# Kernel optimization log

Hardware: AMD Instinct MI355X
Metric: run time of the kernel (lower is better)

## Reference

```python
import jax, jax.numpy as jnp
import numpy as np

B, N, C = 16, 8192, 384   # batch, points, feature dim
G, M = 512, 32            # num_group (FPS centers), group_size (KNN k)


def setup_inputs() -> dict:
    key = jax.random.key(0)
    k1, k2 = jax.random.split(key)
    xyz = jax.random.normal(k1, (B, N, 3), dtype=jnp.float32)
    features = jax.random.normal(k2, (B, N, C), dtype=jnp.float32)
    return {"xyz": xyz, "features": features}


def _fps(xyz, n_samples):
    """Farthest point sampling, deterministic start at index 0 (matches CUDA op).
    xyz: [B, N, 3] -> idx: [B, n_samples] int32."""
    b, n, _ = xyz.shape
    big = jnp.asarray(1e10, xyz.dtype)

    def step(carry, _):
        min_dist, farthest = carry
        centroid = jnp.take_along_axis(xyz, farthest[:, None, None], axis=1)  # [B,1,3]
        d = jnp.sum((xyz - centroid) ** 2, axis=-1)                            # [B,N]
        min_dist = jnp.minimum(min_dist, d)
        nxt = jnp.argmax(min_dist, axis=-1).astype(jnp.int32)
        return (min_dist, nxt), farthest

    init = (jnp.full((b, n), big, xyz.dtype), jnp.zeros((b,), jnp.int32))
    _, idxs = jax.lax.scan(step, init, None, length=n_samples)  # [G, B]
    return jnp.transpose(idxs)  # [B, G]


def _knn_idx(ref, query, k):
    """Indices of k nearest ref points for each query. ref [B,N,3], query [B,G,3] -> [B,G,k]."""
    d = (jnp.sum(query ** 2, -1)[..., None]
         + jnp.sum(ref ** 2, -1)[:, None, :]
         - 2.0 * jnp.einsum('bgd,bnd->bgn', query, ref))  # [B,G,N]
    _, idx = jax.lax.top_k(-d, k)
    return idx


def reference(xyz, features):
    fps_idx = _fps(xyz, G)                                        # [B,G]
    center = jnp.take_along_axis(xyz, fps_idx[..., None], axis=1)  # [B,G,3]
    idx = _knn_idx(xyz, center, M)                                 # [B,G,M]

    gather = jax.vmap(lambda pts, i: pts[i])                       # per-batch fancy gather
    flat_idx = idx.reshape(B, G * M)
    neighborhood = gather(xyz, flat_idx).reshape(B, G, M, 3)
    feature_group = gather(features, flat_idx).reshape(B, G, M, C)
    neighborhood = neighborhood - center[:, :, None, :]
    return neighborhood, center, feature_group
```

## Files before the change

### kernel.cpp

```cpp
#include <hip/hip_runtime.h>
#include <math.h>

#define BATCH 16
#define NPTS  8192
#define FEATC 384
#define NG    512
#define KM    32

#define OUT0_OFF 0
#define OUT1_OFF (BATCH * NG * KM * 3)
#define OUT2_OFF (OUT1_OFF + BATCH * NG * 3)

#pragma clang fp contract(off)

typedef float f32x2 __attribute__((ext_vector_type(2)));

template <int CTRL>
__device__ __forceinline__ unsigned long long dpp_u64(unsigned long long k) {
    unsigned lo = (unsigned)k, hi = (unsigned)(k >> 32);
    lo = (unsigned)__builtin_amdgcn_update_dpp((int)lo, (int)lo, CTRL, 0xF, 0xF, false);
    hi = (unsigned)__builtin_amdgcn_update_dpp((int)hi, (int)hi, CTRL, 0xF, 0xF, false);
    return ((unsigned long long)hi << 32) | lo;
}

__device__ __forceinline__ unsigned long long wave_max_u64(unsigned long long k) {
    unsigned long long o;
    o = dpp_u64<0x111>(k); if (o > k) k = o;
    o = dpp_u64<0x112>(k); if (o > k) k = o;
    o = dpp_u64<0x114>(k); if (o > k) k = o;
    o = dpp_u64<0x118>(k); if (o > k) k = o;
    o = dpp_u64<0x142>(k); if (o > k) k = o;
    o = dpp_u64<0x143>(k); if (o > k) k = o;
    return k;
}

__device__ __forceinline__ unsigned long long wave_min_u64(unsigned long long k) {
    unsigned long long o;
    o = dpp_u64<0x111>(k); if (o < k) k = o;
    o = dpp_u64<0x112>(k); if (o < k) k = o;
    o = dpp_u64<0x114>(k); if (o < k) k = o;
    o = dpp_u64<0x118>(k); if (o < k) k = o;
    o = dpp_u64<0x142>(k); if (o < k) k = o;
    o = dpp_u64<0x143>(k); if (o < k) k = o;
    return k;
}

__device__ __forceinline__ unsigned long long min16_u64(const unsigned long long* k) {
    unsigned long long t8[8];
#pragma unroll
    for (int i = 0; i < 8; ++i) t8[i] = k[i] < k[i + 8] ? k[i] : k[i + 8];
    unsigned long long t4[4];
#pragma unroll
    for (int i = 0; i < 4; ++i) t4[i] = t8[i] < t8[i + 4] ? t8[i] : t8[i + 4];
    unsigned long long a = t4[0] < t4[2] ? t4[0] : t4[2];
    unsigned long long b = t4[1] < t4[3] ? t4[1] : t4[3];
    return a < b ? a : b;
}

__global__ void init_progress(int* progress) {
    if (threadIdx.x < BATCH)
        __hip_atomic_store(&progress[threadIdx.x], 0,
                           __ATOMIC_RELAXED, __HIP_MEMORY_SCOPE_AGENT);
}

__global__ __launch_bounds__(512) void group_kernel(const float* __restrict__ xyz,
                                                    const float* __restrict__ features,
                                                    float* __restrict__ out0,
                                                    float* __restrict__ out1,
                                                    float* __restrict__ out2,
                                                    int* __restrict__ progress) {
#pragma clang fp contract(off)
    __shared__ unsigned long long sk[2][8];
    __shared__ int   sidx[KM];
    __shared__ float scst[24];

    const int tid  = threadIdx.x;
    const int lane = tid & 63;
    const int wid  = tid >> 6;

    if (blockIdx.x < BATCH) {
        __builtin_amdgcn_s_setprio(3);
        const int b = blockIdx.x;
        const float* xb = xyz + (size_t)b * NPTS * 3;
        float* co = out1 + (size_t)b * NG * 3;

        f32x2 X[8], Y[8], Z[8], MD[8];
#pragma unroll
        for (int j = 0; j < 8; ++j) {
            int p0 = tid + 1024 * j;
            int p1 = p0 + 512;
            X[j]  = (f32x2){xb[p0 * 3 + 0], xb[p1 * 3 + 0]};
            Y[j]  = (f32x2){xb[p0 * 3 + 1], xb[p1 * 3 + 1]};
            Z[j]  = (f32x2){xb[p0 * 3 + 2], xb[p1 * 3 + 2]};
            MD[j] = (f32x2){1e10f, 1e10f};
        }

        int far = 0;
        for (int g = 0; g < NG; ++g) {
            const float cx = xb[far * 3 + 0];
            const float cy = xb[far * 3 + 1];
            const float cz = xb[far * 3 + 2];
            if (tid == 0) {
                scst[(g & 7) * 3 + 0] = cx;
                scst[(g & 7) * 3 + 1] = cy;
                scst[(g & 7) * 3 + 2] = cz;
            }
            const f32x2 cx2 = (f32x2){cx, cx};
            const f32x2 cy2 = (f32x2){cy, cy};
            const f32x2 cz2 = (f32x2){cz, cz};

#pragma unroll
            for (int j = 0; j < 8; ++j) {
                f32x2 dx = X[j] - cx2;
                f32x2 dy = Y[j] - cy2;
                f32x2 dz = Z[j] - cz2;
                f32x2 d  = (dx * dx + dy * dy) + dz * dz;
                MD[j] = __builtin_elementwise_min(MD[j], d);
            }
            f32x2 a0 = __builtin_elementwise_max(MD[0], MD[1]);
            f32x2 a1 = __builtin_elementwise_max(MD[2], MD[3]);
            f32x2 a2 = __builtin_elementwise_max(MD[4], MD[5]);
            f32x2 a3 = __builtin_elementwise_max(MD[6], MD[7]);
            f32x2 b0 = __builtin_elementwise_max(a0, a1);
            f32x2 b1 = __builtin_elementwise_max(a2, a3);
            f32x2 c0 = __builtin_elementwise_max(b0, b1);
            float lmax = fmaxf(c0.x, c0.y);

            unsigned candX = 0xFFFFFFFFu, candY = 0xFFFFFFFFu;
#pragma unroll
            for (int j = 7; j >= 0; --j) {
                if (MD[j].y == lmax) candY = (unsigned)(tid + 1024 * j + 512);
                if (MD[j].x == lmax) candX = (unsigned)(tid + 1024 * j);
            }
            unsigned cand = candX < candY ? candX : candY;

            unsigned long long key =
                ((unsigned long long)__float_as_uint(lmax) << 32) | (unsigned)(~cand);
            key = wave_max_u64(key);

            const int par = g & 1;
            if (lane == 63) sk[par][wid] = key;
            __syncthreads();

            unsigned long long m0 = sk[par][0] > sk[par][1] ? sk[par][0] : sk[par][1];
            unsigned long long m1 = sk[par][2] > sk[par][3] ? sk[par][2] : sk[par][3];
            unsigned long long m2 = sk[par][4] > sk[par][5] ? sk[par][4] : sk[par][5];
            unsigned long long m3 = sk[par][6] > sk[par][7] ? sk[par][6] : sk[par][7];
            unsigned long long ma = m0 > m1 ? m0 : m1;
            unsigned long long mb = m2 > m3 ? m2 : m3;
            unsigned long long gk = ma > mb ? ma : mb;
            far = (int)(~(unsigned)gk);

            if ((g & 7) == 7) {
                if (tid < 24) co[(g - 7) * 3 + tid] = scst[tid];
                if (tid == 0)
                    __hip_atomic_store(&progress[b], g + 1,
                                       __ATOMIC_RELEASE, __HIP_MEMORY_SCOPE_AGENT);
            }
        }
        return;
    }

    const int i = blockIdx.x - BATCH;
    const int b = i & 15;
    const int g = i >> 4;
    const int bgrow = b * NG + g;

    if (tid == 0) {
        while ((int)__hip_atomic_load(&progress[b], __ATOMIC_ACQUIRE,
                                      __HIP_MEMORY_SCOPE_AGENT) < g + 1)
            __builtin_amdgcn_s_sleep(32);
        unsigned* co = (unsigned*)out1 + (size_t)bgrow * 3;
        scst[0] = __uint_as_float(__hip_atomic_load(co + 0, __ATOMIC_RELAXED,
                                                    __HIP_MEMORY_SCOPE_AGENT));
        scst[1] = __uint_as_float(__hip_atomic_load(co + 1, __ATOMIC_RELAXED,
                                                    __HIP_MEMORY_SCOPE_AGENT));
        scst[2] = __uint_as_float(__hip_atomic_load(co + 2, __ATOMIC_RELAXED,
                                                    __HIP_MEMORY_SCOPE_AGENT));
    }
    __syncthreads();

    const float cx = scst[0], cy = scst[1], cz = scst[2];
    const float q2 = (cx * cx + cy * cy) + cz * cz;

    const float* xb = xyz + (size_t)b * NPTS * 3;

    unsigned long long k[16];
#pragma unroll
    for (int j = 0; j < 16; ++j) {
        int p = tid + (j << 9);
        float rx = xb[p * 3 + 0];
        float ry = xb[p * 3 + 1];
        float rz = xb[p * 3 + 2];
        float r2 = (rx * rx + ry * ry) + rz * rz;
        float dot = fmaf(cz, rz, fmaf(cy, ry, cx * rx));
        float d = (q2 + r2) - 2.0f * dot;
        unsigned u = __float_as_uint(d);
        u ^= ((unsigned)((int)u >> 31)) | 0x80000000u;
        k[j] = ((unsigned long long)u << 32) | (unsigned)p;
    }

    unsigned long long lv = min16_u64(k);
    unsigned long long wkey = wave_min_u64(lv);
    if (lane == 63) sk[0][wid] = wkey;
    __syncthreads();

    for (int kk = 0; kk < KM; ++kk) {
        const int par = kk & 1;
        const int nxt = par ^ 1;
        unsigned long long m0 = sk[par][0] < sk[par][1] ? sk[par][0] : sk[par][1];
        unsigned long long m1 = sk[par][2] < sk[par][3] ? sk[par][2] : sk[par][3];
        unsigned long long m2 = sk[par][4] < sk[par][5] ? sk[par][4] : sk[par][5];
        unsigned long long m3 = sk[par][6] < sk[par][7] ? sk[par][6] : sk[par][7];
        unsigned long long ma = m0 < m1 ? m0 : m1;
        unsigned long long mb = m2 < m3 ? m2 : m3;
        unsigned long long gk = ma < mb ? ma : mb;
        const unsigned pt = (unsigned)gk;
        const int wwave = (int)((pt & 511u) >> 6);

        if (wid == wwave) {
            if ((pt & 511u) == (unsigned)tid) {
                sidx[kk] = (int)pt;
                const unsigned jw = pt >> 9;
#pragma unroll
                for (int j = 0; j < 16; ++j) {
                    if ((unsigned)j == jw) k[j] = ~0ULL;
                }
                lv = min16_u64(k);
            }
            wkey = wave_min_u64(lv);
            if (lane == 63) sk[nxt][wid] = wkey;
        } else {
            if (lane == 63) sk[nxt][wid] = wkey;
        }
        __syncthreads();
    }

    if (tid < 96) {
        int m = tid / 3;
        int c = tid - 3 * m;
        int p = sidx[m];
        float v = xb[p * 3 + c] - scst[c];
        out0[((size_t)bgrow * KM + m) * 3 + c] = v;
    }

    const float4* fb = (const float4*)(features + (size_t)b * NPTS * FEATC);
    float4*       ob = (float4*)(out2 + (size_t)bgrow * KM * FEATC);
#pragma unroll
    for (int r = 0; r < 6; ++r) {
        int flat = tid + (r << 9);
        int m  = flat / 96;
        int c4 = flat - 96 * m;
        float4 v = fb[(size_t)sidx[m] * 96 + c4];
        ob[(size_t)m * 96 + c4] = v;
    }
}

extern "C" void kernel_launch(void* const* d_in, const int* in_sizes, int n_in,
                              void* d_out, int out_size, void* d_ws, size_t ws_size,
                              hipStream_t stream) {
    const float* xyz      = (const float*)d_in[0];
    const float* features = (const float*)d_in[1];
    float* out  = (float*)d_out;
    float* out0 = out + OUT0_OFF;
    float* out1 = out + OUT1_OFF;
    float* out2 = out + OUT2_OFF;

    int* progress = (int*)d_ws;

    init_progress<<<1, 64, 0, stream>>>(progress);
    group_kernel<<<BATCH + BATCH * NG, 512, 0, stream>>>(xyz, features,
                                                         out0, out1, out2,
                                                         progress);
}
```

Baseline: 700.8 us.

## Carry winning point coordinates through FPS argmax reduction instead of reloading

The FPS loop now carries the candidate point's xyz coordinates alongside the argmax key through the DPP wave reduction and the cross-wave LDS reduction. This removes the dependent global load of the next centroid at the start of each of the serial iterations. The cost is extra DPP moves and LDS traffic per step. Separately, the KNN distance computation is packed into two-wide float vectors so it can use packed FP32 math.

```diff
diff --git a/kernel.cpp b/kernel.cpp
--- a/kernel.cpp
+++ b/kernel.cpp
@@ -16,32 +16,49 @@
 typedef float f32x2 __attribute__((ext_vector_type(2)));
 
 template <int CTRL>
-__device__ __forceinline__ unsigned long long dpp_u64(unsigned long long k) {
+__device__ __forceinline__ int dpp1(int x) {
+    return __builtin_amdgcn_update_dpp(x, x, CTRL, 0xF, 0xF, false);
+}
+
+template <int CTRL>
+__device__ __forceinline__ void argmax_step(unsigned long long& k,
+                                            float& x, float& y, float& z) {
     unsigned lo = (unsigned)k, hi = (unsigned)(k >> 32);
-    lo = (unsigned)__builtin_amdgcn_update_dpp((int)lo, (int)lo, CTRL, 0xF, 0xF, false);
-    hi = (unsigned)__builtin_amdgcn_update_dpp((int)hi, (int)hi, CTRL, 0xF, 0xF, false);
-    return ((unsigned long long)hi << 32) | lo;
-}
-
-__device__ __forceinline__ unsigned long long wave_max_u64(unsigned long long k) {
-    unsigned long long o;
-    o = dpp_u64<0x111>(k); if (o > k) k = o;
-    o = dpp_u64<0x112>(k); if (o > k) k = o;
-    o = dpp_u64<0x114>(k); if (o > k) k = o;
-    o = dpp_u64<0x118>(k); if (o > k) k = o;
-    o = dpp_u64<0x142>(k); if (o > k) k = o;
-    o = dpp_u64<0x143>(k); if (o > k) k = o;
-    return k;
+    unsigned nlo = (unsigned)dpp1<CTRL>((int)lo);
+    unsigned nhi = (unsigned)dpp1<CTRL>((int)hi);
+    int nx = dpp1<CTRL>(__float_as_int(x));
+    int ny = dpp1<CTRL>(__float_as_int(y));
+    int nz = dpp1<CTRL>(__float_as_int(z));
+    unsigned long long nk = ((unsigned long long)nhi << 32) | nlo;
+    if (nk > k) {
+        k = nk;
+        x = __int_as_float(nx);
+        y = __int_as_float(ny);
+        z = __int_as_float(nz);
+    }
+}
+
+__device__ __forceinline__ void wave_argmax_carry(unsigned long long& k,
+                                                  float& x, float& y, float& z) {
+    argmax_step<0x111>(k, x, y, z);
+    argmax_step<0x112>(k, x, y, z);
+    argmax_step<0x114>(k, x, y, z);
+    argmax_step<0x118>(k, x, y, z);
+    argmax_step<0x142>(k, x, y, z);
+    argmax_step<0x143>(k, x, y, z);
 }
 
 __device__ __forceinline__ unsigned long long wave_min_u64(unsigned long long k) {
     unsigned long long o;
-    o = dpp_u64<0x111>(k); if (o < k) k = o;
-    o = dpp_u64<0x112>(k); if (o < k) k = o;
-    o = dpp_u64<0x114>(k); if (o < k) k = o;
-    o = dpp_u64<0x118>(k); if (o < k) k = o;
-    o = dpp_u64<0x142>(k); if (o < k) k = o;
-    o = dpp_u64<0x143>(k); if (o < k) k = o;
+#define STEP(C)                                                                \
+    {                                                                          \
+        unsigned lo = (unsigned)dpp1<C>((int)(unsigned)k);                     \
+        unsigned hi = (unsigned)dpp1<C>((int)(unsigned)(k >> 32));             \
+        o = ((unsigned long long)hi << 32) | lo;                               \
+        if (o < k) k = o;                                                      \
+    }
+    STEP(0x111) STEP(0x112) STEP(0x114) STEP(0x118) STEP(0x142) STEP(0x143)
+#undef STEP
     return k;
 }
 
@@ -71,6 +88,7 @@
                                                     int* __restrict__ progress) {
 #pragma clang fp contract(off)
     __shared__ unsigned long long sk[2][8];
+    __shared__ float4 scd[2][8];
     __shared__ int   sidx[KM];
     __shared__ float scst[24];
 
@@ -94,12 +112,9 @@
             Z[j]  = (f32x2){xb[p0 * 3 + 2], xb[p1 * 3 + 2]};
             MD[j] = (f32x2){1e10f, 1e10f};
         }
-
-        int far = 0;
+        float cx = xb[0], cy = xb[1], cz = xb[2];
+
         for (int g = 0; g < NG; ++g) {
-            const float cx = xb[far * 3 + 0];
-            const float cy = xb[far * 3 + 1];
-            const float cz = xb[far * 3 + 2];
             if (tid == 0) {
                 scst[(g & 7) * 3 + 0] = cx;
                 scst[(g & 7) * 3 + 1] = cy;
@@ -126,30 +141,46 @@
             f32x2 c0 = __builtin_elementwise_max(b0, b1);
             float lmax = fmaxf(c0.x, c0.y);
 
-            unsigned candX = 0xFFFFFFFFu, candY = 0xFFFFFFFFu;
+            unsigned cand = 0xFFFFFFFFu;
+            float bx = 0.f, by = 0.f, bz = 0.f;
 #pragma unroll
             for (int j = 7; j >= 0; --j) {
-                if (MD[j].y == lmax) candY = (unsigned)(tid + 1024 * j + 512);
-                if (MD[j].x == lmax) candX = (unsigned)(tid + 1024 * j);
-            }
-            unsigned cand = candX < candY ? candX : candY;
+                if (MD[j].y == lmax) {
+                    cand = (unsigned)(tid + 1024 * j + 512);
+                    bx = X[j].y; by = Y[j].y; bz = Z[j].y;
+                }
+                if (MD[j].x == lmax) {
+                    cand = (unsigned)(tid + 1024 * j);
+                    bx = X[j].x; by = Y[j].x; bz = Z[j].x;
+                }
+            }
 
             unsigned long long key =
                 ((unsigned long long)__float_as_uint(lmax) << 32) | (unsigned)(~cand);
-            key = wave_max_u64(key);
+            wave_argmax_carry(key, bx, by, bz);
 
             const int par = g & 1;
-            if (lane == 63) sk[par][wid] = key;
+            if (lane == 63) {
+                sk[par][wid] = key;
+                scd[par][wid] = (float4){bx, by, bz, 0.f};
+            }
             __syncthreads();
 
-            unsigned long long m0 = sk[par][0] > sk[par][1] ? sk[par][0] : sk[par][1];
-            unsigned long long m1 = sk[par][2] > sk[par][3] ? sk[par][2] : sk[par][3];
-            unsigned long long m2 = sk[par][4] > sk[par][5] ? sk[par][4] : sk[par][5];
-            unsigned long long m3 = sk[par][6] > sk[par][7] ? sk[par][6] : sk[par][7];
-            unsigned long long ma = m0 > m1 ? m0 : m1;
-            unsigned long long mb = m2 > m3 ? m2 : m3;
-            unsigned long long gk = ma > mb ? ma : mb;
-            far = (int)(~(unsigned)gk);
+            unsigned long long k0 = sk[par][0], k1 = sk[par][1];
+            unsigned long long k2 = sk[par][2], k3 = sk[par][3];
+            unsigned long long k4 = sk[par][4], k5 = sk[par][5];
+            unsigned long long k6 = sk[par][6], k7 = sk[par][7];
+            float4 c0v = scd[par][0], c1v = scd[par][1];
+            float4 c2v = scd[par][2], c3v = scd[par][3];
+            float4 c4v = scd[par][4], c5v = scd[par][5];
+            float4 c6v = scd[par][6], c7v = scd[par][7];
+            if (k1 > k0) { k0 = k1; c0v = c1v; }
+            if (k3 > k2) { k2 = k3; c2v = c3v; }
+            if (k5 > k4) { k4 = k5; c4v = c5v; }
+            if (k7 > k6) { k6 = k7; c6v = c7v; }
+            if (k2 > k0) { k0 = k2; c0v = c2v; }
+            if (k6 > k4) { k4 = k6; c4v = c6v; }
+            if (k4 > k0) { k0 = k4; c0v = c4v; }
 
             if ((g & 7) == 7) {
                 if (tid < 24) co[(g - 7) * 3 + tid] = scst[tid];
@@ -157,6 +188,7 @@
                     __hip_atomic_store(&progress[b], g + 1,
                                        __ATOMIC_RELEASE, __HIP_MEMORY_SCOPE_AGENT);
             }
+            cx = c0v.x; cy = c0v.y; cz = c0v.z;
         }
         return;
     }
@@ -182,22 +214,32 @@
 
     const float cx = scst[0], cy = scst[1], cz = scst[2];
     const float q2 = (cx * cx + cy * cy) + cz * cz;
+    const f32x2 cx2 = (f32x2){cx, cx};
+    const f32x2 cy2 = (f32x2){cy, cy};
+    const f32x2 cz2 = (f32x2){cz, cz};
+    const f32x2 q22 = (f32x2){q2, q2};
+    const f32x2 two = (f32x2){2.0f, 2.0f};
 
     const float* xb = xyz + (size_t)b * NPTS * 3;
 
     unsigned long long k[16];
 #pragma unroll
-    for (int j = 0; j < 16; ++j) {
-        int p = tid + (j << 9);
-        float rx = xb[p * 3 + 0];
-        float ry = xb[p * 3 + 1];
-        float rz = xb[p * 3 + 2];
-        float r2 = (rx * rx + ry * ry) + rz * rz;
-        float dot = fmaf(cz, rz, fmaf(cy, ry, cx * rx));
-        float d = (q2 + r2) - 2.0f * dot;
-        unsigned u = __float_as_uint(d);
-        u ^= ((unsigned)((int)u >> 31)) | 0x80000000u;
-        k[j] = ((unsigned long long)u << 32) | (unsigned)p;
+    for (int i2 = 0; i2 < 8; ++i2) {
+        int p0 = tid + (2 * i2) * 512;
+        int p1 = p0 + 512;
+        f32x2 rx = (f32x2){xb[p0 * 3 + 0], xb[p1 * 3 + 0]};
+        f32x2 ry = (f32x2){xb[p0 * 3 + 1], xb[p1 * 3 + 1]};
+        f32x2 rz = (f32x2){xb[p0 * 3 + 2], xb[p1 * 3 + 2]};
+        f32x2 r2 = (rx * rx + ry * ry) + rz * rz;
+        f32x2 dot = __builtin_elementwise_fma(
+            cz2, rz, __builtin_elementwise_fma(cy2, ry, cx2 * rx));
+        f32x2 d = (q22 + r2) - two * dot;
+        unsigned u0 = __float_as_uint(d.x);
+        u0 ^= ((unsigned)((int)u0 >> 31)) | 0x80000000u;
+        unsigned u1 = __float_as_uint(d.y);
+        u1 ^= ((unsigned)((int)u1 >> 31)) | 0x80000000u;
+        k[2 * i2]     = ((unsigned long long)u0 << 32) | (unsigned)p0;
+        k[2 * i2 + 1] = ((unsigned long long)u1 << 32) | (unsigned)p1;
     }
 
     unsigned long long lv = min16_u64(k);
```

New measurement: 998.3 us. 42.4% more time.
